# Performance work log

Hardware: AMD Instinct MI355X
Metric: run time of the kernel (lower is better)

Reference implementation:

```python
import jax, jax.numpy as jnp
import numpy as np

DIM = 128
N_NODES = 100000
N_EDGES = 1600000


def setup_inputs() -> dict:
    key = jax.random.key(0)
    ks = jax.random.split(key, 9)
    x1 = jax.random.normal(ks[0], (N_NODES, DIM), dtype=jnp.float32)
    x2 = jax.random.normal(ks[1], (N_NODES, DIM), dtype=jnp.float32)
    edge_index = jax.random.randint(ks[2], (2, N_EDGES), 0, N_NODES, dtype=jnp.int64)
    # make_mlp(2*dim, dim, 1, layers=3): Linear(256,128)+ReLU, Linear(128,128)+ReLU, Linear(128,1)
    def lin(k, fan_in, fan_out):
        bound = 1.0 / np.sqrt(fan_in)
        kw, kb = jax.random.split(k)
        W = jax.random.uniform(kw, (fan_in, fan_out), jnp.float32, -bound, bound)
        b = jax.random.uniform(kb, (fan_out,), jnp.float32, -bound, bound)
        return W, b
    W1, b1 = lin(ks[3], 2 * DIM, DIM)
    W2, b2 = lin(ks[4], DIM, DIM)
    W3, b3 = lin(ks[5], DIM, 1)
    return {"x1": x1, "x2": x2, "edge_index": edge_index,
            "W1": W1, "b1": b1, "W2": W2, "b2": b2, "W3": W3, "b3": b3}


def reference(x1, x2, edge_index, W1, b1, W2, b2, W3, b3):
    # Gather endpoints per edge: [E, dim] each
    xs = x1[edge_index[0]]
    xt = x2[edge_index[1]]
    pair = jnp.concatenate([xs, xt], axis=-1)  # [E, 2*dim]
    h = jax.nn.relu(pair @ W1 + b1)            # [E, dim]
    h = jax.nn.relu(h @ W2 + b2)               # [E, dim]
    return h @ W3 + b3                         # [E, 1]
```

## Files before the change

kernel.cpp:

```cpp
#include <hip/hip_runtime.h>
#include <cstdint>

#define DIM 128
#define MTILE 64
#define PAIR_LD 264
#define H_LD 136

typedef __bf16 v8bf __attribute__((ext_vector_type(8)));
typedef _Float16 v8hf __attribute__((ext_vector_type(8)));
typedef float v16f __attribute__((ext_vector_type(16)));

static __device__ __forceinline__ unsigned int f2bf_pack(float a, float b) {
  union { float f; unsigned u; } x, y; x.f = a; y.f = b;
  unsigned lo = (x.u + 0x7FFFu + ((x.u >> 16) & 1u)) >> 16;
  unsigned hi = (y.u + 0x7FFFu + ((y.u >> 16) & 1u)) >> 16;
  return lo | (hi << 16);
}
static __device__ __forceinline__ unsigned short f2bf(float a) {
  union { float f; unsigned u; } x; x.f = a;
  return (unsigned short)((x.u + 0x7FFFu + ((x.u >> 16) & 1u)) >> 16);
}
static __device__ __forceinline__ unsigned short f2h(float a) {
  union { _Float16 h; unsigned short u; } c; c.h = (_Float16)a; return c.u;
}
static __device__ __forceinline__ float bfhi2f(unsigned int hi16) {
  union { unsigned u; float f; } c; c.u = hi16; return c.f;
}

__global__ __launch_bounds__(256) void prep_w(
    const float* __restrict__ W1, const float* __restrict__ W2,
    unsigned short* __restrict__ W1t, unsigned short* __restrict__ W2t,
    int w2_f16) {
  int i = blockIdx.x * 256 + threadIdx.x;
  if (i < 32768) {
    int n = i >> 8, k = i & 255;
    W1t[i] = f2bf(W1[k * 128 + n]);
  } else if (i < 49152) {
    int j = i - 32768;
    int n = j >> 7, k = j & 127;
    float v = W2[k * 128 + n];
    W2t[j] = w2_f16 ? f2h(v) : f2bf(v);
  }
}

__global__ __launch_bounds__(256, 4) void node_precompute(
    const float* __restrict__ x1, const float* __restrict__ x2,
    const unsigned short* __restrict__ W1t, const float* __restrict__ b1,
    unsigned short* __restrict__ y1c, unsigned short* __restrict__ y2c,
    int nnodes)
{
  __shared__ unsigned short sm_x[MTILE * H_LD];
  __shared__ unsigned short sm_y[MTILE * H_LD];

  const int tid = threadIdx.x;
  const int lane = tid & 63;
  const int wv = tid >> 6;
  const int l31 = lane & 31;
  const int l5 = lane >> 5;
  const int nb = wv * 32 + l31;
  const int rslot = tid >> 4;
  const int lane16 = tid & 15;

  const int which = blockIdx.x & 1;
  const int base = (blockIdx.x >> 1) * MTILE;
  const int nvalid = nnodes - base;
  const float* xs = which ? x2 : x1;
  unsigned short* yd = which ? y2c : y1c;

  v8bf B1[8];
#pragma unroll
  for (int kt = 0; kt < 8; ++kt)
    B1[kt] = *reinterpret_cast<const v8bf*>(W1t + nb * 256 + which * 128 + kt * 16 + l5 * 8);
  const float badd = which ? b1[nb] : 0.f;

#pragma unroll
  for (int p = 0; p < 4; ++p) {
    int el = p * 16 + rslot;
    int row = base + el; if (row >= nnodes) row = nnodes - 1;
    const float4* s = reinterpret_cast<const float4*>(xs + (size_t)row * DIM) + lane16 * 2;
    float4 f0 = s[0];
    float4 f1 = s[1];
    uint4 pk;
    pk.x = f2bf_pack(f0.x, f0.y);
    pk.y = f2bf_pack(f0.z, f0.w);
    pk.z = f2bf_pack(f1.x, f1.y);
    pk.w = f2bf_pack(f1.z, f1.w);
    *reinterpret_cast<uint4*>(&sm_x[el * H_LD + lane16 * 8]) = pk;
  }
  __syncthreads();

#pragma unroll
  for (int h = 0; h < 2; ++h) {
    v16f acc;
#pragma unroll
    for (int r = 0; r < 16; ++r) acc[r] = 0.f;
#pragma unroll
    for (int kt = 0; kt < 8; ++kt) {
      v8bf a = *reinterpret_cast<const v8bf*>(&sm_x[(32 * h + l31) * H_LD + kt * 16 + l5 * 8]);
      acc = __builtin_amdgcn_mfma_f32_32x32x16_bf16(a, B1[kt], acc, 0, 0, 0);
    }
#pragma unroll
    for (int r = 0; r < 16; ++r) {
      int m = 32 * h + (r & 3) + 8 * (r >> 2) + 4 * l5;
      sm_y[m * H_LD + nb] = f2h(acc[r] + badd);
    }
  }
  __syncthreads();

#pragma unroll
  for (int p = 0; p < 4; ++p) {
    int el = p * 16 + rslot;
    if (el < nvalid)
      *reinterpret_cast<uint4*>(yd + (size_t)(base + el) * DIM + lane16 * 8) =
          *reinterpret_cast<const uint4*>(&sm_y[el * H_LD + lane16 * 8]);
  }
}

__global__ __launch_bounds__(256, 4) void mlp_edge_y(
    const int* __restrict__ eidx,
    const unsigned short* __restrict__ W2t,
    const float* __restrict__ b2, const float* __restrict__ W3,
    const float* __restrict__ b3, float* __restrict__ out,
    int E, int ntiles,
    const unsigned short* __restrict__ y1c, const unsigned short* __restrict__ y2c)
{
  __shared__ unsigned short sm_h1[MTILE * H_LD];
  __shared__ float sm_part[4 * MTILE];

  const int tid = threadIdx.x;
  const int lane = tid & 63;
  const int wv = tid >> 6;
  const int l31 = lane & 31;
  const int l5 = lane >> 5;
  const int nb = wv * 32 + l31;

  v8hf B2[8];
#pragma unroll
  for (int kt = 0; kt < 8; ++kt)
    B2[kt] = *reinterpret_cast<const v8hf*>(W2t + nb * 128 + kt * 16 + l5 * 8);
  const float bias3 = b3[0];

  float w3r[16], b2r[16];
#pragma unroll
  for (int r = 0; r < 16; ++r) {
    int n2 = wv * 32 + (r & 3) + 8 * (r >> 2) + 4 * l5;
    w3r[r] = W3[n2];
    b2r[r] = b2[n2];
  }

  const int rslot = tid >> 4;
  const int lane16 = tid & 15;

  int idxr[8];
  {
    const int t0 = min((int)blockIdx.x, ntiles - 1);
    const size_t e0 = (size_t)t0 * MTILE;
#pragma unroll
    for (int p = 0; p < 8; ++p) {
      int el = (p & 3) * 16 + rslot;
      idxr[p] = eidx[e0 + el + ((p >= 4) ? (size_t)E : 0)];
    }
  }

  int eprev = -1;

  for (int tile = blockIdx.x; tile < ntiles; tile += gridDim.x) {
    __syncthreads();

    uint4 av[4], bv[4];
#pragma unroll
    for (int p = 0; p < 4; ++p) {
      av[p] = *reinterpret_cast<const uint4*>(y1c + (size_t)idxr[p] * DIM + lane16 * 8);
      bv[p] = *reinterpret_cast<const uint4*>(y2c + (size_t)idxr[p + 4] * DIM + lane16 * 8);
    }

    if (eprev >= 0 && tid < MTILE) {
      float s = sm_part[tid] + sm_part[64 + tid] + sm_part[128 + tid] + sm_part[192 + tid];
      out[eprev + tid] = s + bias3;
    }

#pragma unroll
    for (int p = 0; p < 4; ++p) {
      union { uint4 u; v8hf h; } a, b;
      a.u = av[p]; b.u = bv[p];
      v8hf s = a.h + b.h;
#pragma unroll
      for (int j = 0; j < 8; ++j) s[j] = s[j] > (_Float16)0 ? s[j] : (_Float16)0;
      union { v8hf h; uint4 u; } r; r.h = s;
      int el = p * 16 + rslot;
      *reinterpret_cast<uint4*>(&sm_h1[el * H_LD + lane16 * 8]) = r.u;
    }

    {
      const int tn = min(tile + (int)gridDim.x, ntiles - 1);
      const size_t en = (size_t)tn * MTILE;
#pragma unroll
      for (int p = 0; p < 8; ++p) {
        int el = (p & 3) * 16 + rslot;
        idxr[p] = eidx[en + el + ((p >= 4) ? (size_t)E : 0)];
      }
    }
    __syncthreads();

#pragma unroll
    for (int h = 0; h < 2; ++h) {
      v16f acc;
#pragma unroll
      for (int r = 0; r < 16; ++r) acc[r] = b2r[r];
#pragma unroll
      for (int kt = 0; kt < 8; ++kt) {
        v8hf bf = *reinterpret_cast<const v8hf*>(&sm_h1[(32 * h + l31) * H_LD + kt * 16 + l5 * 8]);
        acc = __builtin_amdgcn_mfma_f32_32x32x16_f16(B2[kt], bf, acc, 0, 0, 0);
      }
      float p = 0.f;
#pragma unroll
      for (int r = 0; r < 16; ++r) p += fmaxf(acc[r], 0.f) * w3r[r];
      p += __shfl_xor(p, 32);
      if (l5 == 0) sm_part[wv * 64 + 32 * h + l31] = p;
    }

    eprev = tile * MTILE;
  }

  __syncthreads();
  if (eprev >= 0 && tid < MTILE) {
    float s = sm_part[tid] + sm_part[64 + tid] + sm_part[128 + tid] + sm_part[192 + tid];
    out[eprev + tid] = s + bias3;
  }
}

__global__ __launch_bounds__(256, 2) void mlp_edge_direct(
    const float* __restrict__ x1, const float* __restrict__ x2,
    const int* __restrict__ eidx,
    const unsigned short* __restrict__ W1t, const unsigned short* __restrict__ W2t,
    const float* __restrict__ b1, const float* __restrict__ b2,
    const float* __restrict__ W3, const float* __restrict__ b3,
    float* __restrict__ out, int E, int ntiles)
{
  __shared__ unsigned short sm_pair[MTILE * PAIR_LD];
  __shared__ unsigned short sm_h1[MTILE * H_LD];
  __shared__ float sm_w3[4 * 36];
  unsigned short* sm_h2 = sm_pair;

  const int tid = threadIdx.x;
  const int lane = tid & 63;
  const int wv = tid >> 6;
  const int l31 = lane & 31;
  const int l5 = lane >> 5;
  const int nb = wv * 32 + l31;

  v8bf B1[16], B2[8];
#pragma unroll
  for (int kt = 0; kt < 16; ++kt)
    B1[kt] = *reinterpret_cast<const v8bf*>(W1t + nb * 256 + kt * 16 + l5 * 8);
#pragma unroll
  for (int kt = 0; kt < 8; ++kt)
    B2[kt] = *reinterpret_cast<const v8bf*>(W2t + nb * 128 + kt * 16 + l5 * 8);
  const float b1v = b1[nb];
  const float b2v = b2[nb];
  const float bias3 = b3[0];
  if (tid < 128) sm_w3[(tid >> 5) * 36 + (tid & 31)] = W3[tid];

  const int rslot = tid >> 4;
  const int lane16 = tid & 15;
  const int part = tid & 3;

  for (int tile = blockIdx.x; tile < ntiles; tile += gridDim.x) {
    __syncthreads();
    const int e0 = tile * MTILE;
#pragma unroll
    for (int p = 0; p < 8; ++p) {
      int rowid = p * 16 + rslot;
      int half = rowid >> 6;
      int el = rowid & 63;
      int node = eidx[e0 + el + (half ? E : 0)];
      const float* src = (half ? x2 : x1) + (size_t)node * DIM + lane16 * 8;
      float4 f0 = *reinterpret_cast<const float4*>(src);
      float4 f1 = *reinterpret_cast<const float4*>(src + 4);
      uint4 pk;
      pk.x = f2bf_pack(f0.x, f0.y);
      pk.y = f2bf_pack(f0.z, f0.w);
      pk.z = f2bf_pack(f1.x, f1.y);
      pk.w = f2bf_pack(f1.z, f1.w);
      *reinterpret_cast<uint4*>(&sm_pair[el * PAIR_LD + half * 128 + lane16 * 8]) = pk;
    }
    __syncthreads();

    v16f acc0, acc1;
#pragma unroll
    for (int r = 0; r < 16; ++r) { acc0[r] = 0.f; acc1[r] = 0.f; }
#pragma unroll
    for (int kt = 0; kt < 16; ++kt) {
      v8bf a0 = *reinterpret_cast<const v8bf*>(&sm_pair[l31 * PAIR_LD + kt * 16 + l5 * 8]);
      v8bf a1 = *reinterpret_cast<const v8bf*>(&sm_pair[(32 + l31) * PAIR_LD + kt * 16 + l5 * 8]);
      acc0 = __builtin_amdgcn_mfma_f32_32x32x16_bf16(a0, B1[kt], acc0, 0, 0, 0);
      acc1 = __builtin_amdgcn_mfma_f32_32x32x16_bf16(a1, B1[kt], acc1, 0, 0, 0);
    }
#pragma unroll
    for (int r = 0; r < 16; ++r) {
      int m = (r & 3) + 8 * (r >> 2) + 4 * l5;
      sm_h1[m * H_LD + nb] = f2bf(fmaxf(acc0[r] + b1v, 0.f));
      sm_h1[(32 + m) * H_LD + nb] = f2bf(fmaxf(acc1[r] + b1v, 0.f));
    }
    __syncthreads();

    v16f c0, c1;
#pragma unroll
    for (int r = 0; r < 16; ++r) { c0[r] = 0.f; c1[r] = 0.f; }
#pragma unroll
    for (int kt = 0; kt < 8; ++kt) {
      v8bf a0 = *reinterpret_cast<const v8bf*>(&sm_h1[l31 * H_LD + kt * 16 + l5 * 8]);
      v8bf a1 = *reinterpret_cast<const v8bf*>(&sm_h1[(32 + l31) * H_LD + kt * 16 + l5 * 8]);
      c0 = __builtin_amdgcn_mfma_f32_32x32x16_bf16(a0, B2[kt], c0, 0, 0, 0);
      c1 = __builtin_amdgcn_mfma_f32_32x32x16_bf16(a1, B2[kt], c1, 0, 0, 0);
    }
#pragma unroll
    for (int r = 0; r < 16; ++r) {
      int m = (r & 3) + 8 * (r >> 2) + 4 * l5;
      sm_h2[m * H_LD + nb] = f2bf(fmaxf(c0[r] + b2v, 0.f));
      sm_h2[(32 + m) * H_LD + nb] = f2bf(fmaxf(c1[r] + b2v, 0.f));
    }
    __syncthreads();

    {
      int el = tid >> 2;
      const unsigned short* hrow = &sm_h2[el * H_LD + part * 32];
      const float* wrow = &sm_w3[part * 36];
      float sum = 0.f;
#pragma unroll
      for (int j = 0; j < 4; ++j) {
        uint4 u = *reinterpret_cast<const uint4*>(hrow + j * 8);
        float4 wa = *reinterpret_cast<const float4*>(wrow + j * 8);
        float4 wb = *reinterpret_cast<const float4*>(wrow + j * 8 + 4);
        sum += bfhi2f(u.x << 16) * wa.x + bfhi2f(u.x & 0xFFFF0000u) * wa.y;
        sum += bfhi2f(u.y << 16) * wa.z + bfhi2f(u.y & 0xFFFF0000u) * wa.w;
        sum += bfhi2f(u.z << 16) * wb.x + bfhi2f(u.z & 0xFFFF0000u) * wb.y;
        sum += bfhi2f(u.w << 16) * wb.z + bfhi2f(u.w & 0xFFFF0000u) * wb.w;
      }
      sum += __shfl_xor(sum, 1, 64);
      sum += __shfl_xor(sum, 2, 64);
      if (part == 0) out[e0 + el] = sum + bias3;
    }
  }
}

extern "C" void kernel_launch(void* const* d_in, const int* in_sizes, int n_in,
                              void* d_out, int out_size, void* d_ws, size_t ws_size,
                              hipStream_t stream) {
  const float* x1 = (const float*)d_in[0];
  const float* x2 = (const float*)d_in[1];
  const int* eidx = (const int*)d_in[2];
  const float* W1 = (const float*)d_in[3];
  const float* b1 = (const float*)d_in[4];
  const float* W2 = (const float*)d_in[5];
  const float* b2 = (const float*)d_in[6];
  const float* W3 = (const float*)d_in[7];
  const float* b3 = (const float*)d_in[8];
  float* out = (float*)d_out;

  int E = in_sizes[2] / 2;
  if (E <= 0) return;
  int ntiles = E / MTILE;
  int nelem = in_sizes[0];
  int nnodes = nelem / DIM;

  unsigned short* W1t = (unsigned short*)d_ws;
  unsigned short* W2t = W1t + 32768;
  size_t woff = 98304;
  size_t need = woff + 2 * (size_t)nelem * 2;
  int use_cache = (ws_size >= need) ? 1 : 0;
  unsigned short* y1c = (unsigned short*)((char*)d_ws + woff);
  unsigned short* y2c = y1c + nelem;

  prep_w<<<192, 256, 0, stream>>>(W1, W2, W1t, W2t, use_cache);

  if (use_cache) {
    int ntn = (nnodes + MTILE - 1) / MTILE;
    node_precompute<<<2 * ntn, 256, 0, stream>>>(x1, x2, W1t, b1, y1c, y2c, nnodes);
    mlp_edge_y<<<2048, 256, 0, stream>>>(eidx, W2t, b2, W3, b3,
                                         out, E, ntiles, y1c, y2c);
  } else {
    mlp_edge_direct<<<512, 256, 0, stream>>>(x1, x2, eidx, W1t, W2t,
                                             b1, b2, W3, b3, out, E, ntiles);
  }
}
```

Measured before the change: 256.3 us.

## Prefetch next tile's gathered rows and move bias/W3 to shared memory

```diff
diff --git a/kernel.cpp b/kernel.cpp
--- a/kernel.cpp
+++ b/kernel.cpp
@@ -126,6 +126,7 @@
 {
   __shared__ unsigned short sm_h1[MTILE * H_LD];
   __shared__ float sm_part[4 * MTILE];
+  __shared__ float2 sm_bw[DIM];
 
   const int tid = threadIdx.x;
   const int lane = tid & 63;
@@ -134,24 +135,23 @@
   const int l5 = lane >> 5;
   const int nb = wv * 32 + l31;
 
+  if (tid < 128) sm_bw[tid] = make_float2(b2[tid], W3[tid]);
+
   v8hf B2[8];
 #pragma unroll
   for (int kt = 0; kt < 8; ++kt)
     B2[kt] = *reinterpret_cast<const v8hf*>(W2t + nb * 128 + kt * 16 + l5 * 8);
   const float bias3 = b3[0];
-
-  float w3r[16], b2r[16];
-#pragma unroll
-  for (int r = 0; r < 16; ++r) {
-    int n2 = wv * 32 + (r & 3) + 8 * (r >> 2) + 4 * l5;
-    w3r[r] = W3[n2];
-    b2r[r] = b2[n2];
-  }
+  const int n2b = wv * 32 + 4 * l5;
 
   const int rslot = tid >> 4;
   const int lane16 = tid & 15;
+  const int G = gridDim.x;
+
+  if (ntiles <= 0) return;
 
   int idxr[8];
+  uint4 av[4], bv[4];
   {
     const int t0 = min((int)blockIdx.x, ntiles - 1);
     const size_t e0 = (size_t)t0 * MTILE;
@@ -160,19 +160,24 @@
       int el = (p & 3) * 16 + rslot;
       idxr[p] = eidx[e0 + el + ((p >= 4) ? (size_t)E : 0)];
     }
-  }
-
-  int eprev = -1;
-
-  for (int tile = blockIdx.x; tile < ntiles; tile += gridDim.x) {
-    __syncthreads();
-
-    uint4 av[4], bv[4];
 #pragma unroll
     for (int p = 0; p < 4; ++p) {
       av[p] = *reinterpret_cast<const uint4*>(y1c + (size_t)idxr[p] * DIM + lane16 * 8);
       bv[p] = *reinterpret_cast<const uint4*>(y2c + (size_t)idxr[p + 4] * DIM + lane16 * 8);
     }
+    const int t1 = min((int)blockIdx.x + G, ntiles - 1);
+    const size_t e1 = (size_t)t1 * MTILE;
+#pragma unroll
+    for (int p = 0; p < 8; ++p) {
+      int el = (p & 3) * 16 + rslot;
+      idxr[p] = eidx[e1 + el + ((p >= 4) ? (size_t)E : 0)];
+    }
+  }
+
+  int eprev = -1;
+
+  for (int tile = blockIdx.x; tile < ntiles; tile += G) {
+    __syncthreads();
 
     if (eprev >= 0 && tid < MTILE) {
       float s = sm_part[tid] + sm_part[64 + tid] + sm_part[128 + tid] + sm_part[192 + tid];
@@ -191,8 +196,13 @@
       *reinterpret_cast<uint4*>(&sm_h1[el * H_LD + lane16 * 8]) = r.u;
     }
 
-    {
-      const int tn = min(tile + (int)gridDim.x, ntiles - 1);
+    if (tile + G < ntiles) {
+#pragma unroll
+      for (int p = 0; p < 4; ++p) {
+        av[p] = *reinterpret_cast<const uint4*>(y1c + (size_t)idxr[p] * DIM + lane16 * 8);
+        bv[p] = *reinterpret_cast<const uint4*>(y2c + (size_t)idxr[p + 4] * DIM + lane16 * 8);
+      }
+      const int tn = min(tile + 2 * G, ntiles - 1);
       const size_t en = (size_t)tn * MTILE;
 #pragma unroll
       for (int p = 0; p < 8; ++p) {
@@ -206,7 +216,7 @@
     for (int h = 0; h < 2; ++h) {
       v16f acc;
 #pragma unroll
-      for (int r = 0; r < 16; ++r) acc[r] = b2r[r];
+      for (int r = 0; r < 16; ++r) acc[r] = 0.f;
 #pragma unroll
       for (int kt = 0; kt < 8; ++kt) {
         v8hf bf = *reinterpret_cast<const v8hf*>(&sm_h1[(32 * h + l31) * H_LD + kt * 16 + l5 * 8]);
@@ -214,7 +224,10 @@
       }
       float p = 0.f;
 #pragma unroll
-      for (int r = 0; r < 16; ++r) p += fmaxf(acc[r], 0.f) * w3r[r];
+      for (int r = 0; r < 16; ++r) {
+        float2 bw = sm_bw[n2b + (r & 3) + 8 * (r >> 2)];
+        p += fmaxf(acc[r] + bw.x, 0.f) * bw.y;
+      }
       p += __shfl_xor(p, 32);
       if (l5 == 0) sm_part[wv * 64 + 32 * h + l31] = p;
     }
@@ -377,7 +390,7 @@
   if (use_cache) {
     int ntn = (nnodes + MTILE - 1) / MTILE;
     node_precompute<<<2 * ntn, 256, 0, stream>>>(x1, x2, W1t, b1, y1c, y2c, nnodes);
-    mlp_edge_y<<<2048, 256, 0, stream>>>(eidx, W2t, b2, W3, b3,
+    mlp_edge_y<<<1024, 256, 0, stream>>>(eidx, W2t, b2, W3, b3,
                                          out, E, ntiles, y1c, y2c);
   } else {
     mlp_edge_direct<<<512, 256, 0, stream>>>(x1, x2, eidx, W1t, W2t,
```

Measured after the change: 308.2 us. +20.2%, slower.

## Double edge tile to 128 rows and move b2/W3 into shared memory

Applied to the files above, without the earlier changes.

```diff
diff --git a/kernel.cpp b/kernel.cpp
--- a/kernel.cpp
+++ b/kernel.cpp
@@ -3,6 +3,7 @@
 
 #define DIM 128
 #define MTILE 64
+#define ETILE 128
 #define PAIR_LD 264
 #define H_LD 136
 
@@ -49,8 +50,7 @@
     unsigned short* __restrict__ y1c, unsigned short* __restrict__ y2c,
     int nnodes)
 {
-  __shared__ unsigned short sm_x[MTILE * H_LD];
-  __shared__ unsigned short sm_y[MTILE * H_LD];
+  __shared__ unsigned short sm[MTILE * H_LD];
 
   const int tid = threadIdx.x;
   const int lane = tid & 63;
@@ -85,25 +85,27 @@
     pk.y = f2bf_pack(f0.z, f0.w);
     pk.z = f2bf_pack(f1.x, f1.y);
     pk.w = f2bf_pack(f1.z, f1.w);
-    *reinterpret_cast<uint4*>(&sm_x[el * H_LD + lane16 * 8]) = pk;
+    *reinterpret_cast<uint4*>(&sm[el * H_LD + lane16 * 8]) = pk;
   }
   __syncthreads();
 
-#pragma unroll
-  for (int h = 0; h < 2; ++h) {
-    v16f acc;
-#pragma unroll
-    for (int r = 0; r < 16; ++r) acc[r] = 0.f;
-#pragma unroll
-    for (int kt = 0; kt < 8; ++kt) {
-      v8bf a = *reinterpret_cast<const v8bf*>(&sm_x[(32 * h + l31) * H_LD + kt * 16 + l5 * 8]);
-      acc = __builtin_amdgcn_mfma_f32_32x32x16_bf16(a, B1[kt], acc, 0, 0, 0);
-    }
-#pragma unroll
-    for (int r = 0; r < 16; ++r) {
-      int m = 32 * h + (r & 3) + 8 * (r >> 2) + 4 * l5;
-      sm_y[m * H_LD + nb] = f2h(acc[r] + badd);
-    }
+  v16f acc0, acc1;
+#pragma unroll
+  for (int r = 0; r < 16; ++r) { acc0[r] = 0.f; acc1[r] = 0.f; }
+#pragma unroll
+  for (int kt = 0; kt < 8; ++kt) {
+    v8bf a0 = *reinterpret_cast<const v8bf*>(&sm[l31 * H_LD + kt * 16 + l5 * 8]);
+    v8bf a1 = *reinterpret_cast<const v8bf*>(&sm[(32 + l31) * H_LD + kt * 16 + l5 * 8]);
+    acc0 = __builtin_amdgcn_mfma_f32_32x32x16_bf16(a0, B1[kt], acc0, 0, 0, 0);
+    acc1 = __builtin_amdgcn_mfma_f32_32x32x16_bf16(a1, B1[kt], acc1, 0, 0, 0);
+  }
+  __syncthreads();
+
+#pragma unroll
+  for (int r = 0; r < 16; ++r) {
+    int m = (r & 3) + 8 * (r >> 2) + 4 * l5;
+    sm[m * H_LD + nb] = f2h(acc0[r] + badd);
+    sm[(32 + m) * H_LD + nb] = f2h(acc1[r] + badd);
   }
   __syncthreads();
 
@@ -112,7 +114,7 @@
     int el = p * 16 + rslot;
     if (el < nvalid)
       *reinterpret_cast<uint4*>(yd + (size_t)(base + el) * DIM + lane16 * 8) =
-          *reinterpret_cast<const uint4*>(&sm_y[el * H_LD + lane16 * 8]);
+          *reinterpret_cast<const uint4*>(&sm[el * H_LD + lane16 * 8]);
   }
 }
 
@@ -124,8 +126,9 @@
     int E, int ntiles,
     const unsigned short* __restrict__ y1c, const unsigned short* __restrict__ y2c)
 {
-  __shared__ unsigned short sm_h1[MTILE * H_LD];
-  __shared__ float sm_part[4 * MTILE];
+  __shared__ unsigned short sm_h1[ETILE * H_LD];
+  __shared__ float sm_part[4 * ETILE];
+  __shared__ float2 sm_bw[DIM];
 
   const int tid = threadIdx.x;
   const int lane = tid & 63;
@@ -134,53 +137,49 @@
   const int l5 = lane >> 5;
   const int nb = wv * 32 + l31;
 
+  if (tid < 128) sm_bw[tid] = make_float2(b2[tid], W3[tid]);
+
   v8hf B2[8];
 #pragma unroll
   for (int kt = 0; kt < 8; ++kt)
     B2[kt] = *reinterpret_cast<const v8hf*>(W2t + nb * 128 + kt * 16 + l5 * 8);
   const float bias3 = b3[0];
-
-  float w3r[16], b2r[16];
-#pragma unroll
-  for (int r = 0; r < 16; ++r) {
-    int n2 = wv * 32 + (r & 3) + 8 * (r >> 2) + 4 * l5;
-    w3r[r] = W3[n2];
-    b2r[r] = b2[n2];
-  }
+  const int n2b = wv * 32 + 4 * l5;
 
   const int rslot = tid >> 4;
   const int lane16 = tid & 15;
 
-  int idxr[8];
+  int idxr[16];
   {
     const int t0 = min((int)blockIdx.x, ntiles - 1);
-    const size_t e0 = (size_t)t0 * MTILE;
+    const size_t e0 = (size_t)t0 * ETILE;
+#pragma unroll
+    for (int p = 0; p < 16; ++p) {
+      int el = (p & 7) * 16 + rslot;
+      size_t ge = e0 + el; if (ge >= (size_t)E) ge = E - 1;
+      idxr[p] = eidx[ge + ((p >= 8) ? (size_t)E : 0)];
+    }
+  }
+
+  int eprev = -1;
+
+  for (int tile = blockIdx.x; tile < ntiles; tile += gridDim.x) {
+    __syncthreads();
+
+    uint4 av[8], bv[8];
 #pragma unroll
     for (int p = 0; p < 8; ++p) {
-      int el = (p & 3) * 16 + rslot;
-      idxr[p] = eidx[e0 + el + ((p >= 4) ? (size_t)E : 0)];
-    }
-  }
-
-  int eprev = -1;
-
-  for (int tile = blockIdx.x; tile < ntiles; tile += gridDim.x) {
-    __syncthreads();
-
-    uint4 av[4], bv[4];
-#pragma unroll
-    for (int p = 0; p < 4; ++p) {
       av[p] = *reinterpret_cast<const uint4*>(y1c + (size_t)idxr[p] * DIM + lane16 * 8);
-      bv[p] = *reinterpret_cast<const uint4*>(y2c + (size_t)idxr[p + 4] * DIM + lane16 * 8);
-    }
-
-    if (eprev >= 0 && tid < MTILE) {
-      float s = sm_part[tid] + sm_part[64 + tid] + sm_part[128 + tid] + sm_part[192 + tid];
+      bv[p] = *reinterpret_cast<const uint4*>(y2c + (size_t)idxr[p + 8] * DIM + lane16 * 8);
+    }
+
+    if (eprev >= 0 && tid < ETILE && eprev + tid < E) {
+      float s = sm_part[tid] + sm_part[128 + tid] + sm_part[256 + tid] + sm_part[384 + tid];
       out[eprev + tid] = s + bias3;
     }
 
 #pragma unroll
-    for (int p = 0; p < 4; ++p) {
+    for (int p = 0; p < 8; ++p) {
       union { uint4 u; v8hf h; } a, b;
       a.u = av[p]; b.u = bv[p];
       v8hf s = a.h + b.h;
@@ -193,20 +192,21 @@
 
     {
       const int tn = min(tile + (int)gridDim.x, ntiles - 1);
-      const size_t en = (size_t)tn * MTILE;
-#pragma unroll
-      for (int p = 0; p < 8; ++p) {
-        int el = (p & 3) * 16 + rslot;
-        idxr[p] = eidx[en + el + ((p >= 4) ? (size_t)E : 0)];
+      const size_t en = (size_t)tn * ETILE;
+#pragma unroll
+      for (int p = 0; p < 16; ++p) {
+        int el = (p & 7) * 16 + rslot;
+        size_t ge = en + el; if (ge >= (size_t)E) ge = E - 1;
+        idxr[p] = eidx[ge + ((p >= 8) ? (size_t)E : 0)];
       }
     }
     __syncthreads();
 
 #pragma unroll
-    for (int h = 0; h < 2; ++h) {
+    for (int h = 0; h < 4; ++h) {
       v16f acc;
 #pragma unroll
-      for (int r = 0; r < 16; ++r) acc[r] = b2r[r];
+      for (int r = 0; r < 16; ++r) acc[r] = 0.f;
 #pragma unroll
       for (int kt = 0; kt < 8; ++kt) {
         v8hf bf = *reinterpret_cast<const v8hf*>(&sm_h1[(32 * h + l31) * H_LD + kt * 16 + l5 * 8]);
@@ -214,17 +214,20 @@
       }
       float p = 0.f;
 #pragma unroll
-      for (int r = 0; r < 16; ++r) p += fmaxf(acc[r], 0.f) * w3r[r];
+      for (int r = 0; r < 16; ++r) {
+        float2 bw = sm_bw[n2b + (r & 3) + 8 * (r >> 2)];
+        p += fmaxf(acc[r] + bw.x, 0.f) * bw.y;
+      }
       p += __shfl_xor(p, 32);
-      if (l5 == 0) sm_part[wv * 64 + 32 * h + l31] = p;
-    }
-
-    eprev = tile * MTILE;
+      if (l5 == 0) sm_part[wv * 128 + 32 * h + l31] = p;
+    }
+
+    eprev = tile * ETILE;
   }
 
   __syncthreads();
-  if (eprev >= 0 && tid < MTILE) {
-    float s = sm_part[tid] + sm_part[64 + tid] + sm_part[128 + tid] + sm_part[192 + tid];
+  if (eprev >= 0 && tid < ETILE && eprev + tid < E) {
+    float s = sm_part[tid] + sm_part[128 + tid] + sm_part[256 + tid] + sm_part[384 + tid];
     out[eprev + tid] = s + bias3;
   }
 }
@@ -360,7 +363,6 @@
 
   int E = in_sizes[2] / 2;
   if (E <= 0) return;
-  int ntiles = E / MTILE;
   int nelem = in_sizes[0];
   int nnodes = nelem / DIM;
 
@@ -377,9 +379,12 @@
   if (use_cache) {
     int ntn = (nnodes + MTILE - 1) / MTILE;
     node_precompute<<<2 * ntn, 256, 0, stream>>>(x1, x2, W1t, b1, y1c, y2c, nnodes);
-    mlp_edge_y<<<2048, 256, 0, stream>>>(eidx, W2t, b2, W3, b3,
+    int ntiles = (E + ETILE - 1) / ETILE;
+    int grid = ntiles < 1024 ? ntiles : 1024;
+    mlp_edge_y<<<grid, 256, 0, stream>>>(eidx, W2t, b2, W3, b3,
                                          out, E, ntiles, y1c, y2c);
   } else {
+    int ntiles = E / MTILE;
     mlp_edge_direct<<<512, 256, 0, stream>>>(x1, x2, eidx, W1t, W2t,
                                              b1, b2, W3, b3, out, E, ntiles);
   }
```

New measurement: 305.0 us. +19.0%, slower.

## Double-buffer edge gathers into LDS via async global_load_lds with XOR swizzle

Applied to the files above, without the earlier changes.

```diff
diff --git a/kernel.cpp b/kernel.cpp
--- a/kernel.cpp
+++ b/kernel.cpp
@@ -3,6 +3,7 @@
 
 #define DIM 128
 #define MTILE 64
+#define ETILE 64
 #define PAIR_LD 264
 #define H_LD 136
 
@@ -25,6 +26,12 @@
 }
 static __device__ __forceinline__ float bfhi2f(unsigned int hi16) {
   union { unsigned u; float f; } c; c.u = hi16; return c.f;
+}
+
+static __device__ __forceinline__ void gload16(const void* g, void* l) {
+  __builtin_amdgcn_global_load_lds(
+      (const __attribute__((address_space(1))) unsigned int*)g,
+      (__attribute__((address_space(3))) unsigned int*)l, 16, 0, 0);
 }
 
 __global__ __launch_bounds__(256) void prep_w(
@@ -49,8 +56,7 @@
     unsigned short* __restrict__ y1c, unsigned short* __restrict__ y2c,
     int nnodes)
 {
-  __shared__ unsigned short sm_x[MTILE * H_LD];
-  __shared__ unsigned short sm_y[MTILE * H_LD];
+  __shared__ unsigned short sm[MTILE * H_LD];
 
   const int tid = threadIdx.x;
   const int lane = tid & 63;
@@ -85,25 +91,27 @@
     pk.y = f2bf_pack(f0.z, f0.w);
     pk.z = f2bf_pack(f1.x, f1.y);
     pk.w = f2bf_pack(f1.z, f1.w);
-    *reinterpret_cast<uint4*>(&sm_x[el * H_LD + lane16 * 8]) = pk;
+    *reinterpret_cast<uint4*>(&sm[el * H_LD + lane16 * 8]) = pk;
   }
   __syncthreads();
 
-#pragma unroll
-  for (int h = 0; h < 2; ++h) {
-    v16f acc;
-#pragma unroll
-    for (int r = 0; r < 16; ++r) acc[r] = 0.f;
-#pragma unroll
-    for (int kt = 0; kt < 8; ++kt) {
-      v8bf a = *reinterpret_cast<const v8bf*>(&sm_x[(32 * h + l31) * H_LD + kt * 16 + l5 * 8]);
-      acc = __builtin_amdgcn_mfma_f32_32x32x16_bf16(a, B1[kt], acc, 0, 0, 0);
-    }
-#pragma unroll
-    for (int r = 0; r < 16; ++r) {
-      int m = 32 * h + (r & 3) + 8 * (r >> 2) + 4 * l5;
-      sm_y[m * H_LD + nb] = f2h(acc[r] + badd);
-    }
+  v16f acc0, acc1;
+#pragma unroll
+  for (int r = 0; r < 16; ++r) { acc0[r] = 0.f; acc1[r] = 0.f; }
+#pragma unroll
+  for (int kt = 0; kt < 8; ++kt) {
+    v8bf a0 = *reinterpret_cast<const v8bf*>(&sm[l31 * H_LD + kt * 16 + l5 * 8]);
+    v8bf a1 = *reinterpret_cast<const v8bf*>(&sm[(32 + l31) * H_LD + kt * 16 + l5 * 8]);
+    acc0 = __builtin_amdgcn_mfma_f32_32x32x16_bf16(a0, B1[kt], acc0, 0, 0, 0);
+    acc1 = __builtin_amdgcn_mfma_f32_32x32x16_bf16(a1, B1[kt], acc1, 0, 0, 0);
+  }
+  __syncthreads();
+
+#pragma unroll
+  for (int r = 0; r < 16; ++r) {
+    int m = (r & 3) + 8 * (r >> 2) + 4 * l5;
+    sm[m * H_LD + nb] = f2h(acc0[r] + badd);
+    sm[(32 + m) * H_LD + nb] = f2h(acc1[r] + badd);
   }
   __syncthreads();
 
@@ -112,11 +120,11 @@
     int el = p * 16 + rslot;
     if (el < nvalid)
       *reinterpret_cast<uint4*>(yd + (size_t)(base + el) * DIM + lane16 * 8) =
-          *reinterpret_cast<const uint4*>(&sm_y[el * H_LD + lane16 * 8]);
-  }
-}
-
-__global__ __launch_bounds__(256, 4) void mlp_edge_y(
+          *reinterpret_cast<const uint4*>(&sm[el * H_LD + lane16 * 8]);
+  }
+}
+
+__global__ __launch_bounds__(256, 2) void mlp_edge_y(
     const int* __restrict__ eidx,
     const unsigned short* __restrict__ W2t,
     const float* __restrict__ b2, const float* __restrict__ W3,
@@ -124,8 +132,9 @@
     int E, int ntiles,
     const unsigned short* __restrict__ y1c, const unsigned short* __restrict__ y2c)
 {
-  __shared__ unsigned short sm_h1[MTILE * H_LD];
-  __shared__ float sm_part[4 * MTILE];
+  __shared__ unsigned short sm_y1[2][ETILE][DIM];
+  __shared__ unsigned short sm_y2[2][ETILE][DIM];
+  __shared__ float sm_part[4 * ETILE];
 
   const int tid = threadIdx.x;
   const int lane = tid & 63;
@@ -134,6 +143,8 @@
   const int l5 = lane >> 5;
   const int nb = wv * 32 + l31;
 
+  if (blockIdx.x >= ntiles) return;
+
   v8hf B2[8];
 #pragma unroll
   for (int kt = 0; kt < 8; ++kt)
@@ -150,57 +161,74 @@
 
   const int rslot = tid >> 4;
   const int lane16 = tid & 15;
+  const int G = gridDim.x;
 
   int idxr[8];
   {
-    const int t0 = min((int)blockIdx.x, ntiles - 1);
-    const size_t e0 = (size_t)t0 * MTILE;
+    const size_t e0 = (size_t)blockIdx.x * ETILE;
 #pragma unroll
     for (int p = 0; p < 8; ++p) {
       int el = (p & 3) * 16 + rslot;
       idxr[p] = eidx[e0 + el + ((p >= 4) ? (size_t)E : 0)];
     }
+#pragma unroll
+    for (int p = 0; p < 4; ++p) {
+      gload16(y1c + (size_t)idxr[p] * DIM + lane16 * 8, &sm_y1[0][p * 16 + wv * 4][0]);
+      gload16(y2c + (size_t)idxr[p + 4] * DIM + lane16 * 8, &sm_y2[0][p * 16 + wv * 4][0]);
+    }
+    const int t1 = min((int)blockIdx.x + G, ntiles - 1);
+    const size_t e1 = (size_t)t1 * ETILE;
+#pragma unroll
+    for (int p = 0; p < 8; ++p) {
+      int el = (p & 3) * 16 + rslot;
+      idxr[p] = eidx[e1 + el + ((p >= 4) ? (size_t)E : 0)];
+    }
   }
 
   int eprev = -1;
-
-  for (int tile = blockIdx.x; tile < ntiles; tile += gridDim.x) {
-    __syncthreads();
-
-    uint4 av[4], bv[4];
-#pragma unroll
-    for (int p = 0; p < 4; ++p) {
-      av[p] = *reinterpret_cast<const uint4*>(y1c + (size_t)idxr[p] * DIM + lane16 * 8);
-      bv[p] = *reinterpret_cast<const uint4*>(y2c + (size_t)idxr[p + 4] * DIM + lane16 * 8);
-    }
-
-    if (eprev >= 0 && tid < MTILE) {
+  int cur = 0;
+
+  for (int tile = blockIdx.x; tile < ntiles; tile += G) {
+    asm volatile("s_waitcnt vmcnt(0) lgkmcnt(0)" ::: "memory");
+    __builtin_amdgcn_s_barrier();
+    __builtin_amdgcn_sched_barrier(0);
+
+    if (eprev >= 0 && tid < ETILE) {
       float s = sm_part[tid] + sm_part[64 + tid] + sm_part[128 + tid] + sm_part[192 + tid];
       out[eprev + tid] = s + bias3;
     }
 
 #pragma unroll
     for (int p = 0; p < 4; ++p) {
-      union { uint4 u; v8hf h; } a, b;
-      a.u = av[p]; b.u = bv[p];
+      int el = p * 16 + rslot;
+      uint4 ua = *reinterpret_cast<const uint4*>(&sm_y1[cur][el][lane16 * 8]);
+      uint4 ub = *reinterpret_cast<const uint4*>(&sm_y2[cur][el][lane16 * 8]);
+      union { uint4 u; v8hf h; } a, b; a.u = ua; b.u = ub;
       v8hf s = a.h + b.h;
 #pragma unroll
       for (int j = 0; j < 8; ++j) s[j] = s[j] > (_Float16)0 ? s[j] : (_Float16)0;
       union { v8hf h; uint4 u; } r; r.h = s;
-      int el = p * 16 + rslot;
-      *reinterpret_cast<uint4*>(&sm_h1[el * H_LD + lane16 * 8]) = r.u;
-    }
-
-    {
-      const int tn = min(tile + (int)gridDim.x, ntiles - 1);
-      const size_t en = (size_t)tn * MTILE;
+      *reinterpret_cast<uint4*>(&sm_y1[cur][el][(lane16 * 8) ^ (rslot << 3)]) = r.u;
+    }
+
+    if (tile + G < ntiles) {
+#pragma unroll
+      for (int p = 0; p < 4; ++p) {
+        gload16(y1c + (size_t)idxr[p] * DIM + lane16 * 8, &sm_y1[cur ^ 1][p * 16 + wv * 4][0]);
+        gload16(y2c + (size_t)idxr[p + 4] * DIM + lane16 * 8, &sm_y2[cur ^ 1][p * 16 + wv * 4][0]);
+      }
+      const int tn = min(tile + 2 * G, ntiles - 1);
+      const size_t en = (size_t)tn * ETILE;
 #pragma unroll
       for (int p = 0; p < 8; ++p) {
         int el = (p & 3) * 16 + rslot;
         idxr[p] = eidx[en + el + ((p >= 4) ? (size_t)E : 0)];
       }
     }
-    __syncthreads();
+
+    asm volatile("s_waitcnt lgkmcnt(0)" ::: "memory");
+    __builtin_amdgcn_s_barrier();
+    __builtin_amdgcn_sched_barrier(0);
 
 #pragma unroll
     for (int h = 0; h < 2; ++h) {
@@ -209,7 +237,9 @@
       for (int r = 0; r < 16; ++r) acc[r] = b2r[r];
 #pragma unroll
       for (int kt = 0; kt < 8; ++kt) {
-        v8hf bf = *reinterpret_cast<const v8hf*>(&sm_h1[(32 * h + l31) * H_LD + kt * 16 + l5 * 8]);
+        int row = 32 * h + l31;
+        int col = (kt * 16 + l5 * 8) ^ ((l31 & 15) << 3);
+        v8hf bf = *reinterpret_cast<const v8hf*>(&sm_y1[cur][row][col]);
         acc = __builtin_amdgcn_mfma_f32_32x32x16_f16(B2[kt], bf, acc, 0, 0, 0);
       }
       float p = 0.f;
@@ -219,11 +249,12 @@
       if (l5 == 0) sm_part[wv * 64 + 32 * h + l31] = p;
     }
 
-    eprev = tile * MTILE;
+    eprev = tile * ETILE;
+    cur ^= 1;
   }
 
   __syncthreads();
-  if (eprev >= 0 && tid < MTILE) {
+  if (eprev >= 0 && tid < ETILE) {
     float s = sm_part[tid] + sm_part[64 + tid] + sm_part[128 + tid] + sm_part[192 + tid];
     out[eprev + tid] = s + bias3;
   }
@@ -360,7 +391,6 @@
 
   int E = in_sizes[2] / 2;
   if (E <= 0) return;
-  int ntiles = E / MTILE;
   int nelem = in_sizes[0];
   int nnodes = nelem / DIM;
 
@@ -377,9 +407,12 @@
   if (use_cache) {
     int ntn = (nnodes + MTILE - 1) / MTILE;
     node_precompute<<<2 * ntn, 256, 0, stream>>>(x1, x2, W1t, b1, y1c, y2c, nnodes);
-    mlp_edge_y<<<2048, 256, 0, stream>>>(eidx, W2t, b2, W3, b3,
+    int ntiles = E / ETILE;
+    int grid = ntiles < 512 ? ntiles : 512;
+    mlp_edge_y<<<grid, 256, 0, stream>>>(eidx, W2t, b2, W3, b3,
                                          out, E, ntiles, y1c, y2c);
   } else {
+    int ntiles = E / MTILE;
     mlp_edge_direct<<<512, 256, 0, stream>>>(x1, x2, eidx, W1t, W2t,
                                              b1, b2, W3, b3, out, E, ntiles);
   }
```

Result: no change. 260.7 us (+1.7%).
